# Kernel tuning notes

Hardware: AMD Instinct MI355X
Metric: run time of the kernel (lower is better)

Reference implementation:

```python
import jax, jax.numpy as jnp
import numpy as np

PRECISION = 127.0

def _pwb_quantize(t):
    # Pulse-width binary mapping: clip to [-1, 1] (layer constraint) and
    # quantize to `precision` discrete levels, as PWBMapper realizes weights.
    t = jnp.clip(t, -1.0, 1.0)
    return jnp.round(t * PRECISION) / PRECISION

def setup_inputs() -> dict:
    key = jax.random.key(0)
    k1, k2, k3 = jax.random.split(key, 3)
    B, DIN, DOUT = 4096, 2048, 2048
    x = jax.random.normal(k1, (B, DIN), dtype=jnp.float32)
    # tf.random_normal_initializer default stddev = 0.05
    W = jax.random.normal(k2, (DIN, DOUT), dtype=jnp.float32) * 0.05
    b = jax.random.normal(k3, (DOUT,), dtype=jnp.float32) * 0.05
    return {"x": x, "W": W, "b": b}

def reference(x, W, b):
    # Fused equivalent of the per-sample / per-neuron Python loops:
    # each neuron's PWB step is a dot product with the quantized weight
    # column; the bias neuron adds the quantized bias. Then activation.
    Wq = _pwb_quantize(W)            # [DIN, DOUT]
    bq = _pwb_quantize(b)            # [DOUT]
    y = jnp.einsum('bi,io->bo', x, Wq) + bq
    return jax.nn.relu(y)
```

## Files before the change

kernel.cpp:

```cpp
#include <hip/hip_runtime.h>
#include <hip/hip_bf16.h>
#include <stdint.h>


typedef __attribute__((ext_vector_type(4))) int i32x4;

#define BM 128
#define BN 128
#define BK 64

__device__ __forceinline__ float pwb_clip(float w) {
    return fminf(fmaxf(w, -1.f), 1.f);
}

__device__ __forceinline__ void gl16(const int8_t* g, int8_t* l) {
    __builtin_amdgcn_global_load_lds(
        (const __attribute__((address_space(1))) void*)(g),
        (__attribute__((address_space(3))) void*)(l),
        16, 0, 0);
}

#define WAIT_VM4   asm volatile("s_waitcnt vmcnt(4)" ::: "memory");
#define WAIT_VM0   asm volatile("s_waitcnt vmcnt(0)" ::: "memory");
#define BAR()      __builtin_amdgcn_s_barrier();

__global__ void pwb_prep(const float* __restrict__ x, const float* __restrict__ W,
                         int8_t* __restrict__ xq, int8_t* __restrict__ Wq,
                         float* __restrict__ scales, int DIN, int DOUT, int xblocks) {
    __shared__ int8_t t[32][36];
    const int tid = threadIdx.x;
    if ((int)blockIdx.x < xblocks) {
        const int row = blockIdx.x * 4 + (tid >> 6);
        const int l   = tid & 63;
        const float4* xr = (const float4*)(x + (size_t)row * DIN);
        const int J = DIN >> 8;
        float m = 0.f;
        for (int j = 0; j < J; ++j) {
            float4 v = xr[j * 64 + l];
            m = fmaxf(m, fmaxf(fmaxf(fabsf(v.x), fabsf(v.y)),
                               fmaxf(fabsf(v.z), fabsf(v.w))));
        }
#pragma unroll
        for (int d = 1; d < 64; d <<= 1) m = fmaxf(m, __shfl_xor(m, d));
        const float r = (m > 0.f) ? 127.f / m : 0.f;
        if (l == 0) scales[row] = m / 16129.f;
        uint32_t* o = (uint32_t*)(xq + (size_t)row * DIN);
        for (int j = 0; j < J; ++j) {
            float4 v = xr[j * 64 + l];
            int q0 = (int)rintf(v.x * r), q1 = (int)rintf(v.y * r);
            int q2 = (int)rintf(v.z * r), q3 = (int)rintf(v.w * r);
            uint32_t u = (uint32_t)(q0 & 255) | ((uint32_t)(q1 & 255) << 8) |
                         ((uint32_t)(q2 & 255) << 16) | ((uint32_t)(q3 & 255) << 24);
            o[j * 64 + l] = u;
        }
    } else {
        const int wb = blockIdx.x - xblocks;
        const int gw = DOUT >> 5;
        const int c0 = (wb % gw) * 32;
        const int r0 = (wb / gw) * 32;
        const int tx = tid & 31, ty = tid >> 5;
#pragma unroll
        for (int i = 0; i < 4; ++i) {
            int row = r0 + ty + i * 8;
            float w = W[(size_t)row * DOUT + c0 + tx];
            t[tx][ty + i * 8] = (int8_t)rintf(pwb_clip(w) * 127.f);
        }
        __syncthreads();
        const int lr = tid >> 3, wd = tid & 7;
        uint32_t u = (uint32_t)(uint8_t)t[lr][wd * 4 + 0]
                   | ((uint32_t)(uint8_t)t[lr][wd * 4 + 1] << 8)
                   | ((uint32_t)(uint8_t)t[lr][wd * 4 + 2] << 16)
                   | ((uint32_t)(uint8_t)t[lr][wd * 4 + 3] << 24);
        ((uint32_t*)(Wq + (size_t)(c0 + lr) * DIN + r0))[wd] = u;
    }
}

__global__ __launch_bounds__(256, 2) void pwb_gemmq(
    const int8_t* __restrict__ A,
    const int8_t* __restrict__ Bt,
    const float* __restrict__ scales,
    const float* __restrict__ b,
    float* __restrict__ C,
    int M, int N, int K, int GN, int nwg) {
    __shared__ __align__(16) int8_t lA[4][BM * BK];
    __shared__ __align__(16) int8_t lB[4][BN * BK];

    const int tid = threadIdx.x;
    const int w   = tid >> 6;
    const int l   = tid & 63;
    const int lr  = l & 15;
    const int lk  = l >> 4;

    const int bid = blockIdx.x;
    const int q = nwg >> 3, r = nwg & 7;
    const int xcd = bid & 7, lin = bid >> 3;
    const int wgid = (xcd < r ? xcd * (q + 1) : r * (q + 1) + (xcd - r) * q) + lin;
    const int tm = wgid / GN, tn = wgid % GN;
    const size_t brow = (size_t)tm * BM, bcol = (size_t)tn * BN;

    const int wm = (w >> 1) * 64;
    const int wn = (w & 1) * 64;

    const int s0 = tid, s1 = tid + 256;
    const int r0c = s0 >> 2, k0c = (s0 & 3) ^ ((s0 >> 3) & 3);
    const int r1c = s1 >> 2, k1c = (s1 & 3) ^ ((s1 >> 3) & 3);
    const int8_t* gA0 = A  + (size_t)(brow + r0c) * K + k0c * 16;
    const int8_t* gA1 = A  + (size_t)(brow + r1c) * K + k1c * 16;
    const int8_t* gB0 = Bt + (size_t)(bcol + r0c) * K + k0c * 16;
    const int8_t* gB1 = Bt + (size_t)(bcol + r1c) * K + k1c * 16;

    const int xk    = (lk ^ ((lr >> 1) & 3)) << 4;
    const int offAb = (wm + lr) * 64 + xk;
    const int offBb = (wn + lr) * 64 + xk;

    i32x4 acc[4][4] = {};

    const int T = K / BK;

#define STAGE(buf, ktg)                              \
    gl16(gA0 + (ktg), &lA[buf][w * 1024]);           \
    gl16(gA1 + (ktg), &lA[buf][w * 1024 + 4096]);    \
    gl16(gB0 + (ktg), &lB[buf][w * 1024]);           \
    gl16(gB1 + (ktg), &lB[buf][w * 1024 + 4096]);

#define LOADFRAGS(fa, fb, bi)                                  \
    _Pragma("unroll") for (int mi = 0; mi < 4; ++mi)           \
        fa[mi] = *(const i32x4*)&lA[bi][offAb + mi * 1024];    \
    _Pragma("unroll") for (int nj = 0; nj < 4; ++nj)           \
        fb[nj] = *(const i32x4*)&lB[bi][offBb + nj * 1024];

#define MFMA16(fa, fb)                                         \
    __builtin_amdgcn_s_setprio(1);                             \
    _Pragma("unroll") for (int mi = 0; mi < 4; ++mi)           \
    _Pragma("unroll") for (int nj = 0; nj < 4; ++nj)           \
        acc[mi][nj] = __builtin_amdgcn_mfma_i32_16x16x64_i8(   \
            fa[mi], fb[nj], acc[mi][nj], 0, 0, 0);             \
    __builtin_amdgcn_s_setprio(0);

    STAGE(0, 0)
    STAGE(1, BK)
    WAIT_VM4
    BAR();

    i32x4 aA[4], bA[4], aB[4], bB[4];
    LOADFRAGS(aA, bA, 0)

    int bR = 1, bS = 2;
    int ktg = 2 * BK;
    const int halfIters = (T - 2) >> 1;
    for (int it = 0; it < halfIters; ++it) {
        STAGE(bS, ktg)
        ktg += BK;
        WAIT_VM4
        BAR();
        LOADFRAGS(aB, bB, bR)
        MFMA16(aA, bA)
        bR = (bR + 1) & 3; bS = (bS + 1) & 3;
        STAGE(bS, ktg)
        ktg += BK;
        WAIT_VM4
        BAR();
        LOADFRAGS(aA, bA, bR)
        MFMA16(aB, bB)
        bR = (bR + 1) & 3; bS = (bS + 1) & 3;
    }
    WAIT_VM0
    BAR();
    LOADFRAGS(aB, bB, bR)
    MFMA16(aA, bA)
    MFMA16(aB, bB)

    float bias[4];
#pragma unroll
    for (int nj = 0; nj < 4; ++nj) {
        float bv = b[bcol + wn + nj * 16 + lr];
        bias[nj] = rintf(pwb_clip(bv) * 127.f) * (1.f / 127.f);
    }

    const size_t orow = brow + wm + lk * 4;
    const size_t ocol = bcol + wn + lr;
    float4 scl[4];
#pragma unroll
    for (int mi = 0; mi < 4; ++mi)
        scl[mi] = *(const float4*)&scales[orow + mi * 16];

#pragma unroll
    for (int mi = 0; mi < 4; ++mi) {
        const float s0_ = scl[mi].x, s1_ = scl[mi].y, s2_ = scl[mi].z, s3_ = scl[mi].w;
#pragma unroll
        for (int nj = 0; nj < 4; ++nj) {
            float v0 = fmaf((float)acc[mi][nj][0], s0_, bias[nj]);
            float v1 = fmaf((float)acc[mi][nj][1], s1_, bias[nj]);
            float v2 = fmaf((float)acc[mi][nj][2], s2_, bias[nj]);
            float v3 = fmaf((float)acc[mi][nj][3], s3_, bias[nj]);
            float* cp = &C[(orow + mi * 16) * N + (ocol + nj * 16)];
            cp[0 * N] = fmaxf(v0, 0.f);
            cp[1 * N] = fmaxf(v1, 0.f);
            cp[2 * N] = fmaxf(v2, 0.f);
            cp[3 * N] = fmaxf(v3, 0.f);
        }
    }
#undef STAGE
#undef LOADFRAGS
#undef MFMA16
}

__global__ void pwb_fallback(const float* __restrict__ x, const float* __restrict__ W,
                             const float* __restrict__ b, float* __restrict__ out,
                             int M, int N, int K) {
    __shared__ float sA[16][17];
    __shared__ float sB[16][17];
    int tx = threadIdx.x, ty = threadIdx.y;
    int row = blockIdx.y * 16 + ty;
    int col = blockIdx.x * 16 + tx;
    float acc = 0.f;
    for (int kt = 0; kt < K; kt += 16) {
        sA[ty][tx] = (row < M && kt + tx < K) ? x[(size_t)row * K + kt + tx] : 0.f;
        float w = (kt + ty < K && col < N) ? W[(size_t)(kt + ty) * N + col] : 0.f;
        sB[ty][tx] = rintf(pwb_clip(w) * 127.f) * (1.f / 127.f);
        __syncthreads();
#pragma unroll
        for (int kk = 0; kk < 16; ++kk) acc += sA[ty][kk] * sB[kk][tx];
        __syncthreads();
    }
    if (row < M && col < N) {
        float v = acc + rintf(pwb_clip(b[col]) * 127.f) * (1.f / 127.f);
        out[(size_t)row * N + col] = fmaxf(v, 0.f);
    }
}

extern "C" void kernel_launch(void* const* d_in, const int* in_sizes, int n_in,
                              void* d_out, int out_size, void* d_ws, size_t ws_size,
                              hipStream_t stream) {
    const float* x = (const float*)d_in[0];
    const float* W = (const float*)d_in[1];
    const float* b = (const float*)d_in[2];
    float* out = (float*)d_out;

    const int DOUT = in_sizes[2];
    const int DIN  = in_sizes[1] / DOUT;
    const int M    = in_sizes[0] / DIN;

    size_t need = (size_t)M * DIN + (size_t)DIN * DOUT + (size_t)M * 4;
    const int T = DIN / BK;
    bool fast = (M % BM == 0) && (M % 4 == 0) && (DOUT % BN == 0) &&
                (DIN % 256 == 0) && (T >= 4) && ((T & 1) == 0) &&
                (DOUT % 32 == 0) && (DIN % 32 == 0) && (ws_size >= need);

    if (fast) {
        int8_t* xq = (int8_t*)d_ws;
        int8_t* Wq = xq + (size_t)M * DIN;
        float* scales = (float*)(Wq + (size_t)DIN * DOUT);

        const int xblocks = M / 4;
        const int wblocks = (DOUT / 32) * (DIN / 32);
        pwb_prep<<<xblocks + wblocks, 256, 0, stream>>>(x, W, xq, Wq, scales,
                                                        DIN, DOUT, xblocks);

        const int GM = M / BM, GN = DOUT / BN, nwg = GM * GN;
        pwb_gemmq<<<nwg, 256, 0, stream>>>(xq, Wq, scales, b, out, M, DOUT, DIN, GN, nwg);
    } else {
        dim3 g((DOUT + 15) / 16, (M + 15) / 16), blk(16, 16);
        pwb_fallback<<<g, blk, 0, stream>>>(x, W, b, out, M, DOUT, DIN);
    }
}
```

Measured before the change: 43.24 us.

## Pre-tile int8 operands into MFMA fragment layout and stream B directly to registers

The prep kernel now writes quantized x and W in a 16-row by 64-k tiled layout that matches the MFMA fragment shape. It also caches each x row in shared memory so x is read from global memory once instead of twice. The GEMM loads B fragments straight from global memory into registers, dropping the B shared-memory buffers and their barriers, and only A is staged through LDS with contiguous loads. This cuts LDS traffic and footprint and removes the swizzle addressing, at the cost of more exposed global load latency for B and a new limit of DIN at most 2048.

```diff
diff --git a/kernel.cpp b/kernel.cpp
--- a/kernel.cpp
+++ b/kernel.cpp
@@ -20,23 +20,29 @@
         16, 0, 0);
 }
 
+#define WAIT_VM6   asm volatile("s_waitcnt vmcnt(6)" ::: "memory");
 #define WAIT_VM4   asm volatile("s_waitcnt vmcnt(4)" ::: "memory");
+#define WAIT_VM2   asm volatile("s_waitcnt vmcnt(2)" ::: "memory");
 #define WAIT_VM0   asm volatile("s_waitcnt vmcnt(0)" ::: "memory");
 #define BAR()      __builtin_amdgcn_s_barrier();
 
 __global__ void pwb_prep(const float* __restrict__ x, const float* __restrict__ W,
                          int8_t* __restrict__ xq, int8_t* __restrict__ Wq,
                          float* __restrict__ scales, int DIN, int DOUT, int xblocks) {
-    __shared__ int8_t t[32][36];
+    __shared__ __align__(16) float smem[4 * 2048];
     const int tid = threadIdx.x;
+    const size_t KB = (size_t)(DIN >> 6) << 10;
+
     if ((int)blockIdx.x < xblocks) {
-        const int row = blockIdx.x * 4 + (tid >> 6);
-        const int l   = tid & 63;
+        const int wv = tid >> 6, l = tid & 63;
+        const int row = blockIdx.x * 4 + wv;
         const float4* xr = (const float4*)(x + (size_t)row * DIN);
+        float* xs = smem + wv * 2048;
         const int J = DIN >> 8;
         float m = 0.f;
         for (int j = 0; j < J; ++j) {
             float4 v = xr[j * 64 + l];
+            *(float4*)&xs[j * 256 + l * 4] = v;
             m = fmaxf(m, fmaxf(fmaxf(fabsf(v.x), fabsf(v.y)),
                                fmaxf(fabsf(v.z), fabsf(v.w))));
         }
@@ -44,34 +50,42 @@
         for (int d = 1; d < 64; d <<= 1) m = fmaxf(m, __shfl_xor(m, d));
         const float r = (m > 0.f) ? 127.f / m : 0.f;
         if (l == 0) scales[row] = m / 16129.f;
-        uint32_t* o = (uint32_t*)(xq + (size_t)row * DIN);
+        int8_t* orow_ = xq + (size_t)(row >> 4) * KB + (row & 15) * 64;
         for (int j = 0; j < J; ++j) {
-            float4 v = xr[j * 64 + l];
+            float4 v = *(const float4*)&xs[j * 256 + l * 4];
             int q0 = (int)rintf(v.x * r), q1 = (int)rintf(v.y * r);
             int q2 = (int)rintf(v.z * r), q3 = (int)rintf(v.w * r);
             uint32_t u = (uint32_t)(q0 & 255) | ((uint32_t)(q1 & 255) << 8) |
                          ((uint32_t)(q2 & 255) << 16) | ((uint32_t)(q3 & 255) << 24);
-            o[j * 64 + l] = u;
+            *(uint32_t*)(orow_ + (size_t)(j * 4 + (l >> 4)) * 1024 + (l & 15) * 4) = u;
         }
     } else {
+        int8_t* tq = (int8_t*)smem;
         const int wb = blockIdx.x - xblocks;
-        const int gw = DOUT >> 5;
-        const int c0 = (wb % gw) * 32;
-        const int r0 = (wb / gw) * 32;
-        const int tx = tid & 31, ty = tid >> 5;
+        const int gw = DOUT >> 6;
+        const int c0 = (wb % gw) * 64;
+        const int r0 = (wb / gw) * 64;
+        const int kl = tid >> 4;
+        const int nc = (tid & 15) * 4;
 #pragma unroll
         for (int i = 0; i < 4; ++i) {
-            int row = r0 + ty + i * 8;
-            float w = W[(size_t)row * DOUT + c0 + tx];
-            t[tx][ty + i * 8] = (int8_t)rintf(pwb_clip(w) * 127.f);
+            int k = r0 + kl + i * 16;
+            float4 wv = *(const float4*)&W[(size_t)k * DOUT + c0 + nc];
+            tq[(nc + 0) * 72 + kl + i * 16] = (int8_t)rintf(pwb_clip(wv.x) * 127.f);
+            tq[(nc + 1) * 72 + kl + i * 16] = (int8_t)rintf(pwb_clip(wv.y) * 127.f);
+            tq[(nc + 2) * 72 + kl + i * 16] = (int8_t)rintf(pwb_clip(wv.z) * 127.f);
+            tq[(nc + 3) * 72 + kl + i * 16] = (int8_t)rintf(pwb_clip(wv.w) * 127.f);
         }
         __syncthreads();
-        const int lr = tid >> 3, wd = tid & 7;
-        uint32_t u = (uint32_t)(uint8_t)t[lr][wd * 4 + 0]
-                   | ((uint32_t)(uint8_t)t[lr][wd * 4 + 1] << 8)
-                   | ((uint32_t)(uint8_t)t[lr][wd * 4 + 2] << 16)
-                   | ((uint32_t)(uint8_t)t[lr][wd * 4 + 3] << 24);
-        ((uint32_t*)(Wq + (size_t)(c0 + lr) * DIN + r0))[wd] = u;
+        const int nl = tid >> 2, cc = (tid & 3) * 16;
+        uint32_t u0 = *(const uint32_t*)&tq[nl * 72 + cc + 0];
+        uint32_t u1 = *(const uint32_t*)&tq[nl * 72 + cc + 4];
+        uint32_t u2 = *(const uint32_t*)&tq[nl * 72 + cc + 8];
+        uint32_t u3 = *(const uint32_t*)&tq[nl * 72 + cc + 12];
+        const int n = c0 + nl;
+        uint32_t* dst = (uint32_t*)(Wq + (size_t)(n >> 4) * KB +
+                                    (size_t)(r0 >> 6) * 1024 + (n & 15) * 64 + cc);
+        dst[0] = u0; dst[1] = u1; dst[2] = u2; dst[3] = u3;
     }
 }
 
@@ -83,7 +97,6 @@
     float* __restrict__ C,
     int M, int N, int K, int GN, int nwg) {
     __shared__ __align__(16) int8_t lA[4][BM * BK];
-    __shared__ __align__(16) int8_t lB[4][BN * BK];
 
     const int tid = threadIdx.x;
     const int w   = tid >> 6;
@@ -101,74 +114,71 @@
     const int wm = (w >> 1) * 64;
     const int wn = (w & 1) * 64;
 
-    const int s0 = tid, s1 = tid + 256;
-    const int r0c = s0 >> 2, k0c = (s0 & 3) ^ ((s0 >> 3) & 3);
-    const int r1c = s1 >> 2, k1c = (s1 & 3) ^ ((s1 >> 3) & 3);
-    const int8_t* gA0 = A  + (size_t)(brow + r0c) * K + k0c * 16;
-    const int8_t* gA1 = A  + (size_t)(brow + r1c) * K + k1c * 16;
-    const int8_t* gB0 = Bt + (size_t)(bcol + r0c) * K + k0c * 16;
-    const int8_t* gB1 = Bt + (size_t)(bcol + r1c) * K + k1c * 16;
-
-    const int xk    = (lk ^ ((lr >> 1) & 3)) << 4;
-    const int offAb = (wm + lr) * 64 + xk;
-    const int offBb = (wn + lr) * 64 + xk;
+    const int KT = K >> 6;
+    const size_t KB = (size_t)KT << 10;
+
+    const int8_t* gA[2];
+#pragma unroll
+    for (int i = 0; i < 2; ++i) {
+        int s = tid + 256 * i;
+        gA[i] = A + (size_t)((brow >> 4) + (s >> 6)) * KB + (s & 63) * 16;
+    }
+    const int8_t* pB = Bt + (size_t)((bcol + wn) >> 4) * KB + lr * 64 + lk * 16;
+    const int offA = (wm >> 4) * 1024 + lr * 64 + lk * 16;
 
     i32x4 acc[4][4] = {};
-
-    const int T = K / BK;
-
-#define STAGE(buf, ktg)                              \
-    gl16(gA0 + (ktg), &lA[buf][w * 1024]);           \
-    gl16(gA1 + (ktg), &lA[buf][w * 1024 + 4096]);    \
-    gl16(gB0 + (ktg), &lB[buf][w * 1024]);           \
-    gl16(gB1 + (ktg), &lB[buf][w * 1024 + 4096]);
-
-#define LOADFRAGS(fa, fb, bi)                                  \
-    _Pragma("unroll") for (int mi = 0; mi < 4; ++mi)           \
-        fa[mi] = *(const i32x4*)&lA[bi][offAb + mi * 1024];    \
-    _Pragma("unroll") for (int nj = 0; nj < 4; ++nj)           \
-        fb[nj] = *(const i32x4*)&lB[bi][offBb + nj * 1024];
-
-#define MFMA16(fa, fb)                                         \
-    __builtin_amdgcn_s_setprio(1);                             \
-    _Pragma("unroll") for (int mi = 0; mi < 4; ++mi)           \
-    _Pragma("unroll") for (int nj = 0; nj < 4; ++nj)           \
-        acc[mi][nj] = __builtin_amdgcn_mfma_i32_16x16x64_i8(   \
-            fa[mi], fb[nj], acc[mi][nj], 0, 0, 0);             \
+    i32x4 bS0[4], bS1[4], afr[4];
+
+#define STAGE(buf, t)                                                   \
+    gl16(gA[0] + (size_t)(t) * 1024, &lA[buf][tid * 16]);               \
+    gl16(gA[1] + (size_t)(t) * 1024, &lA[buf][(tid + 256) * 16]);
+
+#define LOADB(set, t)                                                   \
+    _Pragma("unroll") for (int nj = 0; nj < 4; ++nj)                    \
+        set[nj] = *(const i32x4*)(pB + (size_t)nj * KB + (size_t)(t) * 1024);
+
+#define LOADA(buf)                                                      \
+    _Pragma("unroll") for (int mi = 0; mi < 4; ++mi)                    \
+        afr[mi] = *(const i32x4*)&lA[buf][offA + mi * 1024];
+
+#define MFMA16(fb)                                                      \
+    __builtin_amdgcn_s_setprio(1);                                      \
+    _Pragma("unroll") for (int mi = 0; mi < 4; ++mi)                    \
+    _Pragma("unroll") for (int nj = 0; nj < 4; ++nj)                    \
+        acc[mi][nj] = __builtin_amdgcn_mfma_i32_16x16x64_i8(            \
+            afr[mi], fb[nj], acc[mi][nj], 0, 0, 0);                     \
     __builtin_amdgcn_s_setprio(0);
 
     STAGE(0, 0)
-    STAGE(1, BK)
+    LOADB(bS0, 0)
+    STAGE(1, 1)
+    WAIT_VM2
+    BAR();
+
+    const int T = KT;
+    for (int it = 0; it < (T - 2) / 2; ++it) {
+        const int t0 = 2 * it;
+        LOADB(bS1, t0 + 1)
+        STAGE((t0 + 2) & 3, t0 + 2)
+        LOADA(t0 & 3)
+        WAIT_VM6
+        BAR();
+        MFMA16(bS0)
+        LOADB(bS0, t0 + 2)
+        STAGE((t0 + 3) & 3, t0 + 3)
+        LOADA((t0 + 1) & 3)
+        WAIT_VM6
+        BAR();
+        MFMA16(bS1)
+    }
+    LOADB(bS1, T - 1)
+    LOADA((T - 2) & 3)
     WAIT_VM4
     BAR();
-
-    i32x4 aA[4], bA[4], aB[4], bB[4];
-    LOADFRAGS(aA, bA, 0)
-
-    int bR = 1, bS = 2;
-    int ktg = 2 * BK;
-    const int halfIters = (T - 2) >> 1;
-    for (int it = 0; it < halfIters; ++it) {
-        STAGE(bS, ktg)
-        ktg += BK;
-        WAIT_VM4
-        BAR();
-        LOADFRAGS(aB, bB, bR)
-        MFMA16(aA, bA)
-        bR = (bR + 1) & 3; bS = (bS + 1) & 3;
-        STAGE(bS, ktg)
-        ktg += BK;
-        WAIT_VM4
-        BAR();
-        LOADFRAGS(aA, bA, bR)
-        MFMA16(aB, bB)
-        bR = (bR + 1) & 3; bS = (bS + 1) & 3;
-    }
+    MFMA16(bS0)
     WAIT_VM0
-    BAR();
-    LOADFRAGS(aB, bB, bR)
-    MFMA16(aA, bA)
-    MFMA16(aB, bB)
+    LOADA((T - 1) & 3)
+    MFMA16(bS1)
 
     float bias[4];
 #pragma unroll
@@ -201,7 +211,8 @@
         }
     }
 #undef STAGE
-#undef LOADFRAGS
+#undef LOADB
+#undef LOADA
 #undef MFMA16
 }
 
@@ -243,9 +254,9 @@
 
     size_t need = (size_t)M * DIN + (size_t)DIN * DOUT + (size_t)M * 4;
     const int T = DIN / BK;
-    bool fast = (M % BM == 0) && (M % 4 == 0) && (DOUT % BN == 0) &&
-                (DIN % 256 == 0) && (T >= 4) && ((T & 1) == 0) &&
-                (DOUT % 32 == 0) && (DIN % 32 == 0) && (ws_size >= need);
+    bool fast = (M % BM == 0) && (DOUT % BN == 0) &&
+                (DIN % 256 == 0) && (DIN <= 2048) && (T >= 4) && ((T & 1) == 0) &&
+                (ws_size >= need);
 
     if (fast) {
         int8_t* xq = (int8_t*)d_ws;
@@ -253,7 +264,7 @@
         float* scales = (float*)(Wq + (size_t)DIN * DOUT);
 
         const int xblocks = M / 4;
-        const int wblocks = (DOUT / 32) * (DIN / 32);
+        const int wblocks = (DIN / 64) * (DOUT / 64);
         pwb_prep<<<xblocks + wblocks, 256, 0, stream>>>(x, W, xq, Wq, scales,
                                                         DIN, DOUT, xblocks);
 
```

Measured after the change: 40.53 us. 6.3% less time.
